# Kernel tuning notes

Hardware: AMD Instinct MI355X
Metric: run time of the kernel (lower is better)

Reference implementation:

```python
import jax, jax.numpy as jnp
import numpy as np

NUM_HEADS = 16
EPS = 1e-6


def setup_inputs() -> dict:
    key = jax.random.key(0)
    k1, k2, k3 = jax.random.split(key, 3)
    B, S, D = 4, 4096, 1024
    x = jax.random.normal(k1, (B, S, D), dtype=jnp.float32)
    # weights scaled like nn.Linear init (~1/sqrt(fan_in))
    Wqkv = jax.random.normal(k2, (D, 3 * D), dtype=jnp.float32) / np.sqrt(D)
    Wo = jax.random.normal(k3, (D, D), dtype=jnp.float32) / np.sqrt(D)
    return {"x": x, "Wqkv": Wqkv, "Wo": Wo}


def reference(x, Wqkv, Wo):
    B, S, D = x.shape
    H = NUM_HEADS
    hd = D // H
    qkv = x @ Wqkv                                   # [B,S,3D]
    qkv = qkv.reshape(B, S, 3, H, hd).transpose(2, 0, 3, 1, 4)
    Q, K, V = qkv[0], qkv[1], qkv[2]                 # [B,H,S,hd]
    # feature map: elu(x) + 1 (positive)
    Q = jax.nn.elu(Q) + 1.0
    K = jax.nn.elu(K) + 1.0
    # O(N d^2): KV state then Q contraction
    KV = jnp.einsum('bhnd,bhnv->bhdv', K, V)         # [B,H,hd,hd]
    out = jnp.einsum('bhnd,bhdv->bhnv', Q, KV)       # [B,H,S,hd]
    K_sum = K.sum(axis=2)                            # [B,H,hd]
    normalizer = jnp.einsum('bhnd,bhd->bhn', Q, K_sum)[..., None]  # [B,H,S,1]
    out = out / (normalizer + EPS)
    out = out.transpose(0, 2, 1, 3).reshape(B, S, D)
    return out @ Wo
```

## Files before the change

kernel.cpp:

```cpp
#include <hip/hip_runtime.h>

using u16 = unsigned short;
typedef __attribute__((ext_vector_type(8))) short short8;
typedef __attribute__((ext_vector_type(4))) float f32x4;

__device__ __forceinline__ u16 f2bf(float f) {
  unsigned int u = __float_as_uint(f);
  u = (u + 0x7FFFu + ((u >> 16) & 1u)) >> 16;
  return (u16)u;
}

__device__ __forceinline__ void gload16(const void* g, void* l) {
  __builtin_amdgcn_global_load_lds((const __attribute__((address_space(1))) void*)g,
                                   (__attribute__((address_space(3))) void*)l, 16, 0, 0);
}

#define B_ 4
#define S_ 4096
#define D_ 1024
#define H_ 16
#define HD_ 64
#define M_ (B_*S_)
#define N1_ (3*D_)
#define NSPLIT_ 4

#define OFF_XB    0ull
#define OFF_WQKVT (OFF_XB    + (size_t)M_*D_*2)
#define OFF_WOT   (OFF_WQKVT + (size_t)N1_*D_*2)
#define OFF_QBUF  (OFF_WOT   + (size_t)D_*D_*2)
#define OFF_KT    (OFF_QBUF  + (size_t)M_*D_*2)
#define OFF_VT    (OFF_KT    + (size_t)M_*D_*2)
#define OFF_KV    (OFF_VT    + (size_t)M_*D_*2)
#define OFF_KSUM  (OFF_KV    + (size_t)NSPLIT_*64*4096*4)
#define WS_NEEDED (OFF_KSUM  + (size_t)NSPLIT_*64*64*4)

__global__ __launch_bounds__(256) void prep_kernel(const float* __restrict__ x, u16* __restrict__ xb,
                                                   const float* __restrict__ Wqkv, u16* __restrict__ wqkvt,
                                                   const float* __restrict__ Wo, u16* __restrict__ wot)
{
  __shared__ float tile[32][33];
  int bid = blockIdx.x, tid = threadIdx.x;
  if (bid < 16384) {
    int i = bid * 256 + tid;
    float4 v = ((const float4*)x)[i];
    uint2 o;
    o.x = (unsigned)f2bf(v.x) | ((unsigned)f2bf(v.y) << 16);
    o.y = (unsigned)f2bf(v.z) | ((unsigned)f2bf(v.w) << 16);
    ((uint2*)xb)[i] = o;
    return;
  }
  const float* in; u16* out; int R, C, cb, rb;
  if (bid < 19456) {
    int t = bid - 16384;  in = Wqkv; out = wqkvt; R = D_; C = N1_;
    cb = t % 96; rb = t / 96;
  } else {
    int t = bid - 19456;  in = Wo; out = wot; R = D_; C = D_;
    cb = t % 32; rb = t / 32;
  }
  int tx = tid & 31, ty = tid >> 5;
  int c0 = cb * 32, r0 = rb * 32;
#pragma unroll
  for (int i = 0; i < 4; i++)
    tile[ty + i*8][tx] = in[(size_t)(r0 + ty + i*8) * C + c0 + tx];
  __syncthreads();
#pragma unroll
  for (int i = 0; i < 4; i++)
    out[(size_t)(c0 + ty + i*8) * R + r0 + tx] = f2bf(tile[tx][ty + i*8]);
}

__global__ __launch_bounds__(512, 2) void gemm256(
    const u16* __restrict__ A, const u16* __restrict__ Bt,
    float* __restrict__ Cf, u16* __restrict__ qout,
    u16* __restrict__ Kt, u16* __restrict__ Vt,
    int M, int N, int K, int mode)
{
  __shared__ __align__(16) char smem[131072];
  int tid = threadIdx.x;
  int w = tid >> 6, lane = tid & 63;
  int quad = lane >> 4, l16 = lane & 15;
  int wm = w >> 2, wn = w & 3;

  int nwg = gridDim.x * gridDim.y;
  int flat = blockIdx.y * gridDim.x + blockIdx.x;
  int wg = (flat & 7) * (nwg >> 3) + (flat >> 3);
  int bx = wg % gridDim.x, by = wg / gridDim.x;
  int bm = by * 256, bn = bx * 256;

  int prl = lane >> 3;
  int c4  = (lane & 7) ^ prl;
  int r0  = ((w << 3) + prl) * 2 + (c4 >> 2);
  int koff = (c4 & 3) * 8;
  const u16* gA0 = A  + (size_t)(bm + r0) * K + koff;
  const u16* gB0 = Bt + (size_t)(bn + r0) * K + koff;
  size_t rowskip = (size_t)128 * K;
  char* smemc = smem;
  int ldsAw = w * 1024;
  int ldsBw = 65536 + w * 1024;

  int ph = (((l16 & 1) << 2) | quad) ^ ((l16 >> 1) & 7);
  int baseA = wm * 8192 + (l16 >> 1) * 128 + ph * 16;
  int baseB = 65536 + wn * 4096 + (l16 >> 1) * 128 + ph * 16;

  f32x4 acc[8][4];
#pragma unroll
  for (int i = 0; i < 8; i++)
#pragma unroll
    for (int j = 0; j < 4; j++) acc[i][j] = (f32x4)0.0f;

  int nt = K >> 5;

#define STG(tt, slot) {                                                   \
    const u16* a0_ = gA0 + (tt) * 32;                                     \
    const u16* b0_ = gB0 + (tt) * 32;                                     \
    gload16(a0_,           smemc + (slot)*16384 + ldsAw);                 \
    gload16(a0_ + rowskip, smemc + (slot)*16384 + 8192 + ldsAw);          \
    gload16(b0_,           smemc + (slot)*16384 + ldsBw);                 \
    gload16(b0_ + rowskip, smemc + (slot)*16384 + 8192 + ldsBw);          \
  }

#define COMPUTE(slot) {                                                              \
    const char* sb = smemc + (slot) * 16384;                                         \
    short8 bfr[4], af[8];                                                            \
    _Pragma("unroll")                                                                \
    for (int nj = 0; nj < 4; nj++) bfr[nj] = *(const short8*)(sb + baseB + nj*1024); \
    _Pragma("unroll")                                                                \
    for (int mi = 0; mi < 8; mi++) af[mi] = *(const short8*)(sb + baseA + mi*1024);  \
    __builtin_amdgcn_s_setprio(1);                                                   \
    _Pragma("unroll")                                                                \
    for (int mi = 0; mi < 8; mi++)                                                   \
      _Pragma("unroll")                                                              \
      for (int nj = 0; nj < 4; nj++)                                                 \
        acc[mi][nj] = __builtin_amdgcn_mfma_f32_16x16x32_bf16(af[mi], bfr[nj],       \
                                                              acc[mi][nj], 0, 0, 0); \
    __builtin_amdgcn_s_setprio(0);                                                   \
  }

#define WAITBAR(n) {                                                      \
    asm volatile("s_waitcnt vmcnt(" #n ")" ::: "memory");                 \
    __builtin_amdgcn_s_barrier();                                         \
    asm volatile("" ::: "memory");                                        \
  }

  STG(0, 0); STG(1, 1); STG(2, 2);
  WAITBAR(8)

  for (int tb = 0; tb < nt - 4; tb += 4) {
#pragma unroll
    for (int i = 0; i < 4; ++i) {
      int t = tb + i;
      STG(t + 3, ((i + 3) & 3));
      COMPUTE(i)
      WAITBAR(8)
    }
  }

  STG(nt - 1, 3);
  COMPUTE(0)
  WAITBAR(8)
  COMPUTE(1)
  WAITBAR(4)
  COMPUTE(2)
  WAITBAR(0)
  COMPUTE(3)

#undef STG
#undef COMPUTE
#undef WAITBAR

  int colbase = bn + wn * 64;
  if (mode == 0) {
#pragma unroll
    for (int mi = 0; mi < 8; mi++) {
      int row0 = bm + wm * 128 + mi * 16 + quad * 4;
#pragma unroll
      for (int nj = 0; nj < 4; nj++) {
        int col = colbase + nj * 16 + l16;
#pragma unroll
        for (int r = 0; r < 4; r++)
          Cf[(size_t)(row0 + r) * N + col] = acc[mi][nj][r];
      }
    }
  } else {
    int cls = colbase >> 10;
    if (cls == 0) {
#pragma unroll
      for (int mi = 0; mi < 8; mi++) {
        int row0 = bm + wm * 128 + mi * 16 + quad * 4;
#pragma unroll
        for (int nj = 0; nj < 4; nj++) {
          int col = colbase + nj * 16 + l16;
#pragma unroll
          for (int r = 0; r < 4; r++) {
            float v = acc[mi][nj][r];
            v = (v > 0.0f) ? (v + 1.0f) : __expf(v);
            qout[(size_t)(row0 + r) * D_ + col] = f2bf(v);
          }
        }
      }
    } else {
      int b = bm >> 12;
      int h = (colbase & 1023) >> 6;
      u16* dst = (cls == 1 ? Kt : Vt) + (size_t)((b * 16 + h) * 64) * 4096;
      int sb0 = (bm & 4095) + wm * 128;
      bool doElu = (cls == 1);
#pragma unroll
      for (int mi = 0; mi < 8; mi++) {
        int s = sb0 + mi * 16 + quad * 4;
#pragma unroll
        for (int nj = 0; nj < 4; nj++) {
          int d = nj * 16 + l16;
          float v0 = acc[mi][nj][0], v1 = acc[mi][nj][1], v2 = acc[mi][nj][2], v3 = acc[mi][nj][3];
          if (doElu) {
            v0 = (v0 > 0.0f) ? (v0 + 1.0f) : __expf(v0);
            v1 = (v1 > 0.0f) ? (v1 + 1.0f) : __expf(v1);
            v2 = (v2 > 0.0f) ? (v2 + 1.0f) : __expf(v2);
            v3 = (v3 > 0.0f) ? (v3 + 1.0f) : __expf(v3);
          }
          uint2 o;
          o.x = (unsigned)f2bf(v0) | ((unsigned)f2bf(v1) << 16);
          o.y = (unsigned)f2bf(v2) | ((unsigned)f2bf(v3) << 16);
          *(uint2*)(dst + (size_t)d * 4096 + s) = o;
        }
      }
    }
  }
}

__global__ __launch_bounds__(256) void kv_kernel(const u16* __restrict__ Kt,
                                                 const u16* __restrict__ Vt,
                                                 float* __restrict__ KVp,
                                                 float* __restrict__ Ksp)
{
  __shared__ float red[4096];
  __shared__ float redS[64];
  int tid = threadIdx.x;
  int bh = blockIdx.x;
  int ssplit = blockIdx.y;
  int wave = tid >> 6, lane = tid & 63, quad = lane >> 4, l16 = lane & 15;
  int sbase = ssplit * (S_ / NSPLIT_) + wave * (S_ / NSPLIT_ / 4);
  const u16* Kb = Kt + (size_t)bh * 64 * 4096;
  const u16* Vb = Vt + (size_t)bh * 64 * 4096;
  short8 ones;
#pragma unroll
  for (int e = 0; e < 8; ++e) ones[e] = (short)0x3F80;

  for (int i = tid; i < 4096; i += 256) red[i] = 0.0f;
  if (tid < 64) redS[tid] = 0.0f;

  f32x4 acc[4][4], accs[4];
#pragma unroll
  for (int i = 0; i < 4; i++) {
    accs[i] = (f32x4)0.0f;
#pragma unroll
    for (int j = 0; j < 4; j++) acc[i][j] = (f32x4)0.0f;
  }

  for (int kk = 0; kk < S_ / NSPLIT_ / 4 / 32; ++kk) {
    int s = sbase + kk * 32 + quad * 8;
    short8 af[4], bfr[4];
#pragma unroll
    for (int i = 0; i < 4; i++) {
      af[i]  = *(const short8*)(Kb + (size_t)(i*16 + l16) * 4096 + s);
      bfr[i] = *(const short8*)(Vb + (size_t)(i*16 + l16) * 4096 + s);
    }
#pragma unroll
    for (int i = 0; i < 4; i++) {
#pragma unroll
      for (int j = 0; j < 4; j++)
        acc[i][j] = __builtin_amdgcn_mfma_f32_16x16x32_bf16(af[i], bfr[j], acc[i][j], 0, 0, 0);
      accs[i] = __builtin_amdgcn_mfma_f32_16x16x32_bf16(af[i], ones, accs[i], 0, 0, 0);
    }
  }
  __syncthreads();
#pragma unroll
  for (int i = 0; i < 4; i++) {
    int d0 = i*16 + quad*4;
#pragma unroll
    for (int j = 0; j < 4; j++)
#pragma unroll
      for (int r = 0; r < 4; r++)
        atomicAdd(&red[(d0 + r) * 64 + j*16 + l16], acc[i][j][r]);
    if (l16 == 0)
#pragma unroll
      for (int r = 0; r < 4; r++)
        atomicAdd(&redS[d0 + r], accs[i][r]);
  }
  __syncthreads();
  float* dst = KVp + ((size_t)ssplit * 64 + bh) * 4096;
  for (int i = tid; i < 4096; i += 256) dst[i] = red[i];
  if (tid < 64) Ksp[((size_t)ssplit * 64 + bh) * 64 + tid] = redS[tid];
}

__global__ __launch_bounds__(256) void attn_kernel(const u16* __restrict__ qbuf,
                                                   const float* __restrict__ KVp,
                                                   const float* __restrict__ Ksp,
                                                   u16* __restrict__ attn)
{
  __shared__ u16 KVt[64 * 72];
  int tid = threadIdx.x;
  int bh = blockIdx.y;
  int b = bh >> 4, h = bh & 15;
  int s0 = blockIdx.x * 128;
  const float* kvsrc = KVp + (size_t)bh * 4096;
  for (int i = tid; i < 4096; i += 256) {
    float s = kvsrc[i] + kvsrc[i + 64*4096] + kvsrc[i + 2*64*4096] + kvsrc[i + 3*64*4096];
    int d = i >> 6, v = i & 63;
    KVt[v * 72 + d] = f2bf(s);
  }
  __syncthreads();
  int wave = tid >> 6, lane = tid & 63, quad = lane >> 4, l16 = lane & 15;

  const float* kssrc = Ksp + (size_t)bh * 64;
  short8 bks[2];
#pragma unroll
  for (int ks = 0; ks < 2; ++ks)
#pragma unroll
    for (int jj = 0; jj < 8; ++jj) {
      int d = ks*32 + quad*8 + jj;
      float s = kssrc[d] + kssrc[d + 64*64] + kssrc[d + 2*64*64] + kssrc[d + 3*64*64];
      bks[ks][jj] = (short)f2bf(s);
    }

  f32x4 acc[2][4], accn[2];
#pragma unroll
  for (int i = 0; i < 2; i++) {
    accn[i] = (f32x4)0.0f;
#pragma unroll
    for (int j = 0; j < 4; j++) acc[i][j] = (f32x4)0.0f;
  }

#pragma unroll
  for (int ks = 0; ks < 2; ++ks) {
    short8 bfr[4];
#pragma unroll
    for (int j = 0; j < 4; j++)
      bfr[j] = *(const short8*)(&KVt[(j*16 + l16) * 72 + ks*32 + quad*8]);
#pragma unroll
    for (int i = 0; i < 2; i++) {
      int row = s0 + wave * 32 + i * 16 + l16;
      short8 afr = *(const short8*)(qbuf + (size_t)(b * S_ + row) * D_ + h*HD_ + ks*32 + quad*8);
#pragma unroll
      for (int j = 0; j < 4; j++)
        acc[i][j] = __builtin_amdgcn_mfma_f32_16x16x32_bf16(afr, bfr[j], acc[i][j], 0, 0, 0);
      accn[i] = __builtin_amdgcn_mfma_f32_16x16x32_bf16(afr, bks[ks], accn[i], 0, 0, 0);
    }
  }
#pragma unroll
  for (int i = 0; i < 2; i++) {
    int rb = wave * 32 + i * 16 + quad * 4;
#pragma unroll
    for (int j = 0; j < 4; j++) {
      int col = h * HD_ + j * 16 + l16;
#pragma unroll
      for (int r = 0; r < 4; r++) {
        float o = acc[i][j][r] / (accn[i][r] + 1e-6f);
        attn[(size_t)(b * S_ + s0 + rb + r) * D_ + col] = f2bf(o);
      }
    }
  }
}

extern "C" void kernel_launch(void* const* d_in, const int* in_sizes, int n_in,
                              void* d_out, int out_size, void* d_ws, size_t ws_size,
                              hipStream_t stream) {
  const float* x    = (const float*)d_in[0];
  const float* Wqkv = (const float*)d_in[1];
  const float* Wo   = (const float*)d_in[2];
  float* out = (float*)d_out;
  char* ws = (char*)d_ws;
  if (ws_size < WS_NEEDED) return;

  u16*   xb    = (u16*)  (ws + OFF_XB);
  u16*   wqkvt = (u16*)  (ws + OFF_WQKVT);
  u16*   wot   = (u16*)  (ws + OFF_WOT);
  u16*   qbuf  = (u16*)  (ws + OFF_QBUF);
  u16*   kt    = (u16*)  (ws + OFF_KT);
  u16*   vt    = (u16*)  (ws + OFF_VT);
  float* kvp   = (float*)(ws + OFF_KV);
  float* ksp   = (float*)(ws + OFF_KSUM);
  u16*   attnb = (u16*)  (ws + OFF_KT);

  prep_kernel<<<20480, 256, 0, stream>>>(x, xb, Wqkv, wqkvt, Wo, wot);
  gemm256<<<dim3(N1_/256, M_/256), 512, 0, stream>>>(xb, wqkvt, nullptr, qbuf, kt, vt,
                                                     M_, N1_, D_, 1);
  kv_kernel<<<dim3(64, NSPLIT_), 256, 0, stream>>>(kt, vt, kvp, ksp);
  attn_kernel<<<dim3(32, 64), 256, 0, stream>>>(qbuf, kvp, ksp, attnb);
  gemm256<<<dim3(D_/256, M_/256), 512, 0, stream>>>(attnb, wot, out, nullptr, nullptr, nullptr,
                                                    M_, D_, D_, 0);
}
```

Baseline: 331.9 us.

## Split GEMM k-step into two MFMA phases interleaved with staged global loads

Restructures the main GEMM loop so each k-tile is computed in two halves of 4x4 MFMAs. The A and B global-to-LDS prefetches are issued separately between the phases, with extra barriers and explicit lgkmcnt waits around each half. The aim is to hide load issue and LDS reads under MFMA work, in a ping-pong style schedule across waves. In exchange it adds more barriers per step, which could add synchronisation stalls.

```diff
diff --git a/kernel.cpp b/kernel.cpp
--- a/kernel.cpp
+++ b/kernel.cpp
@@ -109,63 +109,81 @@
 
   int nt = K >> 5;
 
-#define STG(tt, slot) {                                                   \
+#define STGA(tt, slot) {                                                  \
     const u16* a0_ = gA0 + (tt) * 32;                                     \
-    const u16* b0_ = gB0 + (tt) * 32;                                     \
     gload16(a0_,           smemc + (slot)*16384 + ldsAw);                 \
     gload16(a0_ + rowskip, smemc + (slot)*16384 + 8192 + ldsAw);          \
+  }
+#define STGB(tt, slot) {                                                  \
+    const u16* b0_ = gB0 + (tt) * 32;                                     \
     gload16(b0_,           smemc + (slot)*16384 + ldsBw);                 \
     gload16(b0_ + rowskip, smemc + (slot)*16384 + 8192 + ldsBw);          \
   }
-
-#define COMPUTE(slot) {                                                              \
-    const char* sb = smemc + (slot) * 16384;                                         \
-    short8 bfr[4], af[8];                                                            \
-    _Pragma("unroll")                                                                \
-    for (int nj = 0; nj < 4; nj++) bfr[nj] = *(const short8*)(sb + baseB + nj*1024); \
-    _Pragma("unroll")                                                                \
-    for (int mi = 0; mi < 8; mi++) af[mi] = *(const short8*)(sb + baseA + mi*1024);  \
-    __builtin_amdgcn_s_setprio(1);                                                   \
-    _Pragma("unroll")                                                                \
-    for (int mi = 0; mi < 8; mi++)                                                   \
-      _Pragma("unroll")                                                              \
-      for (int nj = 0; nj < 4; nj++)                                                 \
-        acc[mi][nj] = __builtin_amdgcn_mfma_f32_16x16x32_bf16(af[mi], bfr[nj],       \
-                                                              acc[mi][nj], 0, 0, 0); \
-    __builtin_amdgcn_s_setprio(0);                                                   \
-  }
-
-#define WAITBAR(n) {                                                      \
-    asm volatile("s_waitcnt vmcnt(" #n ")" ::: "memory");                 \
-    __builtin_amdgcn_s_barrier();                                         \
-    asm volatile("" ::: "memory");                                        \
-  }
-
-  STG(0, 0); STG(1, 1); STG(2, 2);
-  WAITBAR(8)
+#define VM(n) asm volatile("s_waitcnt vmcnt(" #n ")" ::: "memory");
+
+#define STEP(slot, SA, SB, ENDW) {                                                    \
+    const char* sb = smemc + (slot) * 16384;                                          \
+    short8 bfr[4], af[4];                                                             \
+    SA                                                                                \
+    _Pragma("unroll")                                                                 \
+    for (int nj = 0; nj < 4; nj++) bfr[nj] = *(const short8*)(sb + baseB + nj*1024);  \
+    _Pragma("unroll")                                                                 \
+    for (int mi = 0; mi < 4; mi++) af[mi] = *(const short8*)(sb + baseA + mi*1024);   \
+    __builtin_amdgcn_s_barrier();                                                     \
+    asm volatile("s_waitcnt lgkmcnt(0)" ::: "memory");                                \
+    __builtin_amdgcn_sched_barrier(0);                                                \
+    __builtin_amdgcn_s_setprio(1);                                                    \
+    _Pragma("unroll")                                                                 \
+    for (int mi = 0; mi < 4; mi++)                                                    \
+      _Pragma("unroll")                                                               \
+      for (int nj = 0; nj < 4; nj++)                                                  \
+        acc[mi][nj] = __builtin_amdgcn_mfma_f32_16x16x32_bf16(af[mi], bfr[nj],        \
+                                                              acc[mi][nj], 0, 0, 0);  \
+    __builtin_amdgcn_s_setprio(0);                                                    \
+    __builtin_amdgcn_s_barrier();                                                     \
+    SB                                                                                \
+    _Pragma("unroll")                                                                 \
+    for (int mi = 0; mi < 4; mi++) af[mi] = *(const short8*)(sb + baseA + (mi+4)*1024);\
+    __builtin_amdgcn_s_barrier();                                                     \
+    asm volatile("s_waitcnt lgkmcnt(0)" ::: "memory");                                \
+    __builtin_amdgcn_sched_barrier(0);                                                \
+    __builtin_amdgcn_s_setprio(1);                                                    \
+    _Pragma("unroll")                                                                 \
+    for (int mi = 0; mi < 4; mi++)                                                    \
+      _Pragma("unroll")                                                               \
+      for (int nj = 0; nj < 4; nj++)                                                  \
+        acc[mi+4][nj] = __builtin_amdgcn_mfma_f32_16x16x32_bf16(af[mi], bfr[nj],      \
+                                                                acc[mi+4][nj], 0, 0, 0);\
+    __builtin_amdgcn_s_setprio(0);                                                    \
+    ENDW                                                                              \
+    __builtin_amdgcn_s_barrier();                                                     \
+    asm volatile("" ::: "memory");                                                    \
+  }
+
+  STGA(0, 0) STGB(0, 0)
+  STGA(1, 1) STGB(1, 1)
+  STGA(2, 2) STGB(2, 2)
+  VM(8)
+  __builtin_amdgcn_s_barrier();
+  asm volatile("" ::: "memory");
 
   for (int tb = 0; tb < nt - 4; tb += 4) {
 #pragma unroll
     for (int i = 0; i < 4; ++i) {
       int t = tb + i;
-      STG(t + 3, ((i + 3) & 3));
-      COMPUTE(i)
-      WAITBAR(8)
-    }
-  }
-
-  STG(nt - 1, 3);
-  COMPUTE(0)
-  WAITBAR(8)
-  COMPUTE(1)
-  WAITBAR(4)
-  COMPUTE(2)
-  WAITBAR(0)
-  COMPUTE(3)
-
-#undef STG
-#undef COMPUTE
-#undef WAITBAR
+      STEP(i, STGA(t + 3, ((i + 3) & 3)), STGB(t + 3, ((i + 3) & 3)), VM(8))
+    }
+  }
+
+  STEP(0, STGA(nt - 1, 3), STGB(nt - 1, 3), VM(8))
+  STEP(1, , , VM(4))
+  STEP(2, , , VM(0))
+  STEP(3, , , )
+
+#undef STEP
+#undef STGA
+#undef STGB
+#undef VM
 
   int colbase = bn + wn * 64;
   if (mode == 0) {
```

New measurement: 329.4 us. No clear change (-0.7%).

## Add dedicated 128x256 output-projection GEMM with occupancy hints and XCD-aware tile swizzle

Applied to the files above, without the earlier changes.

Replaces the generic 256x256 GEMM for the final output projection with a specialized 128x256 tile kernel using launch_bounds(512,4), double-buffered direct-to-LDS loads, and a block index remap that spreads tiles across chiplets. The smaller tile doubles the number of workgroups (512 vs 256) for better CU utilization on the M=16384, N=1024 GEMM and raises occupancy. The trade-off is lower arithmetic intensity per tile and more redundant loads of A/B.

```diff
diff --git a/kernel.cpp b/kernel.cpp
--- a/kernel.cpp
+++ b/kernel.cpp
@@ -226,6 +226,108 @@
   }
 }
 
+__global__ __launch_bounds__(512, 4) void gemm_op(
+    const u16* __restrict__ A, const u16* __restrict__ Bt,
+    float* __restrict__ Cf, int M, int N, int K)
+{
+  __shared__ __align__(16) char smem[49152];
+  int tid = threadIdx.x;
+  int w = tid >> 6, lane = tid & 63;
+  int quad = lane >> 4, l16 = lane & 15;
+  int wm = w >> 2, wn = w & 3;
+
+  int nwg = gridDim.x * gridDim.y;
+  int flat = blockIdx.y * gridDim.x + blockIdx.x;
+  int wg = (flat & 7) * (nwg >> 3) + (flat >> 3);
+  int bx = wg % gridDim.x, by = wg / gridDim.x;
+  int bm = by * 128, bn = bx * 256;
+
+  int prl = lane >> 3;
+  int c4  = (lane & 7) ^ prl;
+  int r0  = ((w << 3) + prl) * 2 + (c4 >> 2);
+  int koff = (c4 & 3) * 8;
+  const u16* gA0 = A  + (size_t)(bm + r0) * K + koff;
+  const u16* gB0 = Bt + (size_t)(bn + r0) * K + koff;
+  size_t rowskip = (size_t)128 * K;
+  char* smemc = smem;
+  int ldsW = w * 1024;
+
+  int ph = (((l16 & 1) << 2) | quad) ^ ((l16 >> 1) & 7);
+  int baseA0 = wm * 4096 + (l16 >> 1) * 128 + ph * 16;
+  int baseB0 = 16384 + wn * 4096 + (l16 >> 1) * 128 + ph * 16;
+
+  f32x4 acc[4][4];
+#pragma unroll
+  for (int i = 0; i < 4; i++)
+#pragma unroll
+    for (int j = 0; j < 4; j++) acc[i][j] = (f32x4)0.0f;
+
+  int nt = K >> 5;
+
+#define STG(tt, slot) {                                                   \
+    const u16* a0_ = gA0 + (tt) * 32;                                     \
+    const u16* b0_ = gB0 + (tt) * 32;                                     \
+    gload16(a0_,           smemc + (slot)*8192 + ldsW);                   \
+    gload16(b0_,           smemc + 16384 + (slot)*16384 + ldsW);          \
+    gload16(b0_ + rowskip, smemc + 16384 + (slot)*16384 + 8192 + ldsW);   \
+  }
+#define VM(n) asm volatile("s_waitcnt vmcnt(" #n ")" ::: "memory");
+
+#define STEP(slot, STGSTMT, WAITSTMT) {                                              \
+    short8 bfr[4], af[4];                                                            \
+    _Pragma("unroll")                                                                \
+    for (int nj = 0; nj < 4; nj++)                                                   \
+      bfr[nj] = *(const short8*)(smemc + (slot)*16384 + baseB0 + nj*1024);           \
+    _Pragma("unroll")                                                                \
+    for (int mi = 0; mi < 4; mi++)                                                   \
+      af[mi] = *(const short8*)(smemc + (slot)*8192 + baseA0 + mi*1024);             \
+    asm volatile("s_waitcnt lgkmcnt(0)" ::: "memory");                               \
+    __builtin_amdgcn_s_barrier();                                                    \
+    asm volatile("" ::: "memory");                                                   \
+    STGSTMT                                                                          \
+    __builtin_amdgcn_s_setprio(1);                                                   \
+    _Pragma("unroll")                                                                \
+    for (int mi = 0; mi < 4; mi++)                                                   \
+      _Pragma("unroll")                                                              \
+      for (int nj = 0; nj < 4; nj++)                                                 \
+        acc[mi][nj] = __builtin_amdgcn_mfma_f32_16x16x32_bf16(af[mi], bfr[nj],       \
+                                                              acc[mi][nj], 0, 0, 0); \
+    __builtin_amdgcn_s_setprio(0);                                                   \
+    WAITSTMT                                                                         \
+    __builtin_amdgcn_s_barrier();                                                    \
+    asm volatile("" ::: "memory");                                                   \
+  }
+
+  STG(0, 0) STG(1, 1)
+  VM(3)
+  __builtin_amdgcn_s_barrier();
+  asm volatile("" ::: "memory");
+
+  for (int tb = 0; tb < nt - 2; tb += 2) {
+    STEP(0, STG(tb + 2, 0), VM(3))
+    STEP(1, STG(tb + 3, 1), VM(3))
+  }
+  STEP(0, , VM(0))
+  STEP(1, , )
+
+#undef STEP
+#undef STG
+#undef VM
+
+  int colbase = bn + wn * 64;
+#pragma unroll
+  for (int mi = 0; mi < 4; mi++) {
+    int row0 = bm + wm * 64 + mi * 16 + quad * 4;
+#pragma unroll
+    for (int nj = 0; nj < 4; nj++) {
+      int col = colbase + nj * 16 + l16;
+#pragma unroll
+      for (int r = 0; r < 4; r++)
+        Cf[(size_t)(row0 + r) * N + col] = acc[mi][nj][r];
+    }
+  }
+}
+
 __global__ __launch_bounds__(256) void kv_kernel(const u16* __restrict__ Kt,
                                                  const u16* __restrict__ Vt,
                                                  float* __restrict__ KVp,
@@ -385,6 +487,5 @@
                                                      M_, N1_, D_, 1);
   kv_kernel<<<dim3(64, NSPLIT_), 256, 0, stream>>>(kt, vt, kvp, ksp);
   attn_kernel<<<dim3(32, 64), 256, 0, stream>>>(qbuf, kvp, ksp, attnb);
-  gemm256<<<dim3(D_/256, M_/256), 512, 0, stream>>>(attnb, wot, out, nullptr, nullptr, nullptr,
-                                                    M_, D_, D_, 0);
-}
+  gemm_op<<<dim3(D_/256, M_/128), 512, 0, stream>>>(attnb, wot, out, M_, D_, D_);
+}
```

Result: no change. 333.9 us (+0.6%).

## Fold per-head KV state into Wo and drop the attention output pass

Applied to the files above, without the earlier changes.

Uses associativity to precompute per-batch fused weights W_b = blockdiag(KV_h)·Wo, so the final GEMM consumes normalized Q directly. A small qscale kernel divides Q rows in place by their per-head normalizer, replacing the attention kernel that wrote a full attention buffer. This removes one full activation write and read, at the cost of a per-batch weight build and an extra bf16 rounding of the fused weights. The output GEMM now selects its B matrix by batch.

```diff
diff --git a/kernel.cpp b/kernel.cpp
--- a/kernel.cpp
+++ b/kernel.cpp
@@ -8,6 +8,9 @@
   unsigned int u = __float_as_uint(f);
   u = (u + 0x7FFFu + ((u >> 16) & 1u)) >> 16;
   return (u16)u;
+}
+__device__ __forceinline__ float bf2f(u16 v) {
+  return __uint_as_float(((unsigned int)v) << 16);
 }
 
 __device__ __forceinline__ void gload16(const void* g, void* l) {
@@ -33,6 +36,8 @@
 #define OFF_KV    (OFF_VT    + (size_t)M_*D_*2)
 #define OFF_KSUM  (OFF_KV    + (size_t)NSPLIT_*64*4096*4)
 #define WS_NEEDED (OFF_KSUM  + (size_t)NSPLIT_*64*64*4)
+#define OFF_WT    OFF_KT
+#define OFF_KSG   (OFF_KT + (size_t)8*1024*1024)
 
 __global__ __launch_bounds__(256) void prep_kernel(const float* __restrict__ x, u16* __restrict__ xb,
                                                    const float* __restrict__ Wqkv, u16* __restrict__ wqkvt,
@@ -86,12 +91,14 @@
   int bx = wg % gridDim.x, by = wg / gridDim.x;
   int bm = by * 256, bn = bx * 256;
 
+  const u16* Bp = (mode == 2) ? (Bt + ((size_t)(bm >> 12) << 20)) : Bt;
+
   int prl = lane >> 3;
   int c4  = (lane & 7) ^ prl;
   int r0  = ((w << 3) + prl) * 2 + (c4 >> 2);
   int koff = (c4 & 3) * 8;
   const u16* gA0 = A  + (size_t)(bm + r0) * K + koff;
-  const u16* gB0 = Bt + (size_t)(bn + r0) * K + koff;
+  const u16* gB0 = Bp + (size_t)(bn + r0) * K + koff;
   size_t rowskip = (size_t)128 * K;
   char* smemc = smem;
   int ldsAw = w * 1024;
@@ -168,7 +175,7 @@
 #undef WAITBAR
 
   int colbase = bn + wn * 64;
-  if (mode == 0) {
+  if (mode != 1) {
 #pragma unroll
     for (int mi = 0; mi < 8; mi++) {
       int row0 = bm + wm * 128 + mi * 16 + quad * 4;
@@ -291,73 +298,98 @@
   if (tid < 64) Ksp[((size_t)ssplit * 64 + bh) * 64 + tid] = redS[tid];
 }
 
-__global__ __launch_bounds__(256) void attn_kernel(const u16* __restrict__ qbuf,
-                                                   const float* __restrict__ KVp,
-                                                   const float* __restrict__ Ksp,
-                                                   u16* __restrict__ attn)
+__global__ __launch_bounds__(256) void kvw_kernel(const float* __restrict__ KVp,
+                                                  const float* __restrict__ Ksp,
+                                                  const u16* __restrict__ wot,
+                                                  u16* __restrict__ wt,
+                                                  float* __restrict__ ksum)
 {
-  __shared__ u16 KVt[64 * 72];
+  __shared__ u16 kvlds[4096];
   int tid = threadIdx.x;
+  int ct = blockIdx.x;
   int bh = blockIdx.y;
   int b = bh >> 4, h = bh & 15;
-  int s0 = blockIdx.x * 128;
   const float* kvsrc = KVp + (size_t)bh * 4096;
   for (int i = tid; i < 4096; i += 256) {
     float s = kvsrc[i] + kvsrc[i + 64*4096] + kvsrc[i + 2*64*4096] + kvsrc[i + 3*64*4096];
-    int d = i >> 6, v = i & 63;
-    KVt[v * 72 + d] = f2bf(s);
+    kvlds[i] = f2bf(s);
+  }
+  if (ct == 0 && tid < 64) {
+    const float* ks = Ksp + (size_t)bh * 64;
+    ksum[bh * 64 + tid] = ks[tid] + ks[tid + 64*64] + ks[tid + 2*64*64] + ks[tid + 3*64*64];
   }
   __syncthreads();
-  int wave = tid >> 6, lane = tid & 63, quad = lane >> 4, l16 = lane & 15;
-
-  const float* kssrc = Ksp + (size_t)bh * 64;
-  short8 bks[2];
+  int w = tid >> 6, lane = tid & 63, quad = lane >> 4, l16 = lane & 15;
+
+  short8 bfr[2][4];
 #pragma unroll
   for (int ks = 0; ks < 2; ++ks)
 #pragma unroll
-    for (int jj = 0; jj < 8; ++jj) {
-      int d = ks*32 + quad*8 + jj;
-      float s = kssrc[d] + kssrc[d + 64*64] + kssrc[d + 2*64*64] + kssrc[d + 3*64*64];
-      bks[ks][jj] = (short)f2bf(s);
-    }
-
-  f32x4 acc[2][4], accn[2];
-#pragma unroll
-  for (int i = 0; i < 2; i++) {
-    accn[i] = (f32x4)0.0f;
+    for (int nj = 0; nj < 4; ++nj)
+      bfr[ks][nj] = *(const short8*)(&kvlds[(nj*16 + l16) * 64 + ks*32 + quad*8]);
+
+  f32x4 acc[2][4];
+#pragma unroll
+  for (int i = 0; i < 2; i++)
 #pragma unroll
     for (int j = 0; j < 4; j++) acc[i][j] = (f32x4)0.0f;
-  }
-
+
+  int c0 = ct * 128 + w * 32;
 #pragma unroll
   for (int ks = 0; ks < 2; ++ks) {
-    short8 bfr[4];
-#pragma unroll
-    for (int j = 0; j < 4; j++)
-      bfr[j] = *(const short8*)(&KVt[(j*16 + l16) * 72 + ks*32 + quad*8]);
-#pragma unroll
-    for (int i = 0; i < 2; i++) {
-      int row = s0 + wave * 32 + i * 16 + l16;
-      short8 afr = *(const short8*)(qbuf + (size_t)(b * S_ + row) * D_ + h*HD_ + ks*32 + quad*8);
-#pragma unroll
-      for (int j = 0; j < 4; j++)
-        acc[i][j] = __builtin_amdgcn_mfma_f32_16x16x32_bf16(afr, bfr[j], acc[i][j], 0, 0, 0);
-      accn[i] = __builtin_amdgcn_mfma_f32_16x16x32_bf16(afr, bks[ks], accn[i], 0, 0, 0);
-    }
-  }
-#pragma unroll
-  for (int i = 0; i < 2; i++) {
-    int rb = wave * 32 + i * 16 + quad * 4;
-#pragma unroll
-    for (int j = 0; j < 4; j++) {
-      int col = h * HD_ + j * 16 + l16;
-#pragma unroll
-      for (int r = 0; r < 4; r++) {
-        float o = acc[i][j][r] / (accn[i][r] + 1e-6f);
-        attn[(size_t)(b * S_ + s0 + rb + r) * D_ + col] = f2bf(o);
-      }
-    }
-  }
+#pragma unroll
+    for (int mi = 0; mi < 2; ++mi) {
+      short8 af = *(const short8*)(wot + (size_t)(c0 + mi*16 + l16) * 1024 + h*64 + ks*32 + quad*8);
+#pragma unroll
+      for (int nj = 0; nj < 4; ++nj)
+        acc[mi][nj] = __builtin_amdgcn_mfma_f32_16x16x32_bf16(af, bfr[ks][nj], acc[mi][nj], 0, 0, 0);
+    }
+  }
+  u16* dst = wt + ((size_t)b << 20);
+#pragma unroll
+  for (int mi = 0; mi < 2; ++mi) {
+    int c = c0 + mi*16 + quad*4;
+#pragma unroll
+    for (int nj = 0; nj < 4; ++nj) {
+      int hd = h*64 + nj*16 + l16;
+#pragma unroll
+      for (int r = 0; r < 4; ++r)
+        dst[(size_t)(c + r) * 1024 + hd] = f2bf(acc[mi][nj][r]);
+    }
+  }
+}
+
+__global__ __launch_bounds__(256) void qscale_kernel(u16* __restrict__ qbuf,
+                                                     const float* __restrict__ ksum)
+{
+  __shared__ float ks[1024];
+  int tid = threadIdx.x;
+  int blk = blockIdx.x;
+  int b = blk >> 10;
+  for (int i = tid; i < 1024; i += 256) ks[i] = ksum[b * 1024 + i];
+  __syncthreads();
+  int wv = tid >> 6, ln = tid & 63;
+  int s = blk * 4 + wv;
+  u16* row = qbuf + (size_t)s * 1024 + ln * 16;
+  short8 qa = *(const short8*)row;
+  short8 qb = *(const short8*)(row + 8);
+  int h4 = (ln >> 2) * 64 + (ln & 3) * 16;
+  float p = 0.0f;
+#pragma unroll
+  for (int j = 0; j < 8; ++j) p += bf2f((u16)qa[j]) * ks[h4 + j];
+#pragma unroll
+  for (int j = 0; j < 8; ++j) p += bf2f((u16)qb[j]) * ks[h4 + 8 + j];
+  p += __shfl_xor(p, 1);
+  p += __shfl_xor(p, 2);
+  float inv = 1.0f / (p + 1e-6f);
+  short8 oa, ob;
+#pragma unroll
+  for (int j = 0; j < 8; ++j) {
+    oa[j] = (short)f2bf(bf2f((u16)qa[j]) * inv);
+    ob[j] = (short)f2bf(bf2f((u16)qb[j]) * inv);
+  }
+  *(short8*)row = oa;
+  *(short8*)(row + 8) = ob;
 }
 
 extern "C" void kernel_launch(void* const* d_in, const int* in_sizes, int n_in,
@@ -378,13 +410,15 @@
   u16*   vt    = (u16*)  (ws + OFF_VT);
   float* kvp   = (float*)(ws + OFF_KV);
   float* ksp   = (float*)(ws + OFF_KSUM);
-  u16*   attnb = (u16*)  (ws + OFF_KT);
+  u16*   wt    = (u16*)  (ws + OFF_WT);
+  float* ksg   = (float*)(ws + OFF_KSG);
 
   prep_kernel<<<20480, 256, 0, stream>>>(x, xb, Wqkv, wqkvt, Wo, wot);
   gemm256<<<dim3(N1_/256, M_/256), 512, 0, stream>>>(xb, wqkvt, nullptr, qbuf, kt, vt,
                                                      M_, N1_, D_, 1);
   kv_kernel<<<dim3(64, NSPLIT_), 256, 0, stream>>>(kt, vt, kvp, ksp);
-  attn_kernel<<<dim3(32, 64), 256, 0, stream>>>(qbuf, kvp, ksp, attnb);
-  gemm256<<<dim3(D_/256, M_/256), 512, 0, stream>>>(attnb, wot, out, nullptr, nullptr, nullptr,
-                                                    M_, D_, D_, 0);
-}
+  kvw_kernel<<<dim3(8, 64), 256, 0, stream>>>(kvp, ksp, wot, wt, ksg);
+  qscale_kernel<<<4096, 256, 0, stream>>>(qbuf, ksg);
+  gemm256<<<dim3(D_/256, M_/256), 512, 0, stream>>>(qbuf, wt, out, nullptr, nullptr, nullptr,
+                                                    M_, D_, D_, 2);
+}
```

New measurement: 334.5 us. Within noise of the previous version (+0.8%).
